# Optimization experiments

Measured on AMD Instinct MI355X. Metric: run time of the kernel, lower is better.

Reference implementation:

```python
import jax, jax.numpy as jnp
import numpy as np
from jax import lax

WINDOW_SIZE = 11
SIGMA = 1.5
C1 = 0.01 ** 2
C2 = 0.03 ** 2
EPS_DEN = 1e-12
EPS_CLAMP = 1e-6


def _gaussian_window(size=WINDOW_SIZE, sigma=SIGMA):
    xs = jnp.arange(size, dtype=jnp.float32) - size // 2
    g = jnp.exp(-(xs ** 2) / (2.0 * sigma ** 2))
    g = g / g.sum()
    w = g[:, None] * g[None, :]
    w = w / w.sum()  # already ~1; matches torch's redundant renorm
    return w  # [k, k]


def _depthwise_filter(x, window):
    # x: [B, C, H, W]; depthwise 'SAME' conv (stride 1, odd k == pad k//2)
    ch = x.shape[1]
    k = window.shape[0]
    w = jnp.broadcast_to(window[None, None], (ch, 1, k, k)).astype(x.dtype)
    return lax.conv_general_dilated(
        x, w, window_strides=(1, 1), padding='SAME',
        feature_group_count=ch,
        dimension_numbers=('NCHW', 'OIHW', 'NCHW'))


def setup_inputs() -> dict:
    key = jax.random.key(0)
    kx, ky = jax.random.split(key)
    B, C, H, W = 32, 1, 512, 512
    x = jax.random.uniform(kx, (B, C, H, W), dtype=jnp.float32)
    y = jax.random.uniform(ky, (B, C, H, W), dtype=jnp.float32)
    return {"x": x, "y": y}


def reference(x, y):
    window = _gaussian_window().astype(x.dtype)
    mu_x = _depthwise_filter(x, window)
    mu_y = _depthwise_filter(y, window)
    sigma_x = _depthwise_filter(x * x, window) - mu_x * mu_x
    sigma_y = _depthwise_filter(y * y, window) - mu_y * mu_y
    sigma_xy = _depthwise_filter(x * y, window) - mu_x * mu_y
    num = (2.0 * mu_x * mu_y + C1) * (2.0 * sigma_xy + C2)
    den = (mu_x * mu_x + mu_y * mu_y + C1) * (sigma_x + sigma_y + C2)
    ssim_map = num / (den + EPS_DEN)
    ssim_map = jnp.clip(ssim_map, -1.0 + EPS_CLAMP, 1.0 - EPS_CLAMP)
    return 1.0 - jnp.mean(ssim_map)
```

## Files before the change

kernel.cpp:

```cpp
#include <hip/hip_runtime.h>

#define IMG    512
#define TW     32
#define TH     64
#define R      5
#define KW     11
#define HB_H   (TH + 2*R)
#define HB_W   33
#define GX     (IMG / TW)
#define GY     (IMG / TH)
#define NBATCH 32
#define NB     (GX * GY * NBATCH)

#define C1f 0.0001f
#define C2f 0.0009f

__device__ __forceinline__ void make_window(float* w) {
    float s = 0.f;
#pragma unroll
    for (int i = 0; i < KW; ++i) {
        float d = (float)(i - R);
        w[i] = expf(-(d * d) * (1.0f / (2.0f * 1.5f * 1.5f)));
        s += w[i];
    }
    float inv = 1.0f / s;
#pragma unroll
    for (int i = 0; i < KW; ++i) w[i] *= inv;
}

__global__ __launch_bounds__(256, 3) void ssim_tile_kernel(
    const float* __restrict__ x, const float* __restrict__ y,
    float* __restrict__ partials)
{
    __shared__ float4 hb4[HB_H][HB_W];
    __shared__ float  hb1[HB_H][HB_W];
    __shared__ float  red[4];

    float w[KW];
    make_window(w);

    const int tc = blockIdx.x;
    const int tr = blockIdx.y;
    const int b  = blockIdx.z;
    const int tid = threadIdx.x;

    const size_t imgBase = (size_t)b * IMG * IMG;
    const int gr0 = tr * TH - R;

    for (int it = tid; it < HB_H * 8; it += 256) {
        const int rr = it >> 3;
        const int g  = it & 7;
        const int gr = gr0 + rr;
        const bool rowok = (gr >= 0) && (gr < IMG);
        const int grc = rowok ? gr : 0;
        const float4* rx = (const float4*)(x + imgBase + (size_t)grc * IMG);
        const float4* ry = (const float4*)(y + imgBase + (size_t)grc * IMG);

        const int c4 = tc * 8 + g - 2;
        float fx[20], fy[20];
#pragma unroll
        for (int i = 0; i < 5; ++i) {
            int ci = c4 + i;
            bool ok = rowok && (ci >= 0) && (ci < IMG / 4);
            int cic = min(max(ci, 0), IMG / 4 - 1);
            float4 vx = rx[cic];
            float4 vy = ry[cic];
            float m = ok ? 1.f : 0.f;
            fx[4*i+0] = vx.x * m; fx[4*i+1] = vx.y * m;
            fx[4*i+2] = vx.z * m; fx[4*i+3] = vx.w * m;
            fy[4*i+0] = vy.x * m; fy[4*i+1] = vy.y * m;
            fy[4*i+2] = vy.z * m; fy[4*i+3] = vy.w * m;
        }
        float xx[14], yy[14], xy[14];
#pragma unroll
        for (int t = 0; t < 14; ++t) {
            float px = fx[3 + t], py = fy[3 + t];
            xx[t] = px * px; yy[t] = py * py; xy[t] = px * py;
        }
#pragma unroll
        for (int k = 0; k < 4; ++k) {
            float ax = 0.f, ay = 0.f, axx = 0.f, ayy = 0.f, axy = 0.f;
#pragma unroll
            for (int t = 0; t < KW; ++t) {
                float wt = w[t];
                int j = k + t;
                ax  += wt * fx[3 + j];
                ay  += wt * fy[3 + j];
                axx += wt * xx[j];
                ayy += wt * yy[j];
                axy += wt * xy[j];
            }
            hb4[rr][4*g + k] = make_float4(ax, ay, axx, ayy);
            hb1[rr][4*g + k] = axy;
        }
    }
    __syncthreads();

    const int tx = tid & 31;
    const int ty = tid >> 5;
    const int r0 = ty * 8;

    float a0[8], a1[8], a2[8], a3[8], a4[8];
#pragma unroll
    for (int k = 0; k < 8; ++k) { a0[k]=0.f; a1[k]=0.f; a2[k]=0.f; a3[k]=0.f; a4[k]=0.f; }

#pragma unroll
    for (int t = 0; t < 18; ++t) {
        float4 v4 = hb4[r0 + t][tx];
        float  v1 = hb1[r0 + t][tx];
#pragma unroll
        for (int k = 0; k < 8; ++k) {
            if (t - k >= 0 && t - k < KW) {
                float wt = w[t - k];
                a0[k] += wt * v4.x;
                a1[k] += wt * v4.y;
                a2[k] += wt * v4.z;
                a3[k] += wt * v4.w;
                a4[k] += wt * v1;
            }
        }
    }

    float lsum = 0.f;
#pragma unroll
    for (int k = 0; k < 8; ++k) {
        float mux = a0[k], muy = a1[k];
        float sxx = a2[k] - mux * mux;
        float syy = a3[k] - muy * muy;
        float sxy = a4[k] - mux * muy;
        float num = (2.f * mux * muy + C1f) * (2.f * sxy + C2f);
        float den = (mux * mux + muy * muy + C1f) * (sxx + syy + C2f);
        float ssim = num / (den + 1e-12f);
        ssim = fminf(fmaxf(ssim, -1.f + 1e-6f), 1.f - 1e-6f);
        lsum += ssim;
    }

#pragma unroll
    for (int off = 32; off > 0; off >>= 1)
        lsum += __shfl_down(lsum, off, 64);
    if ((tid & 63) == 0) red[tid >> 6] = lsum;
    __syncthreads();
    if (tid == 0) {
        float s = red[0] + red[1] + red[2] + red[3];
        partials[((size_t)b * GY + tr) * GX + tc] = s;
    }
}

__global__ __launch_bounds__(256) void ssim_finalize(
    const float* __restrict__ partials, float* __restrict__ out)
{
    __shared__ float red[4];
    float s = 0.f;
    for (int i = threadIdx.x; i < NB; i += 256) s += partials[i];
#pragma unroll
    for (int off = 32; off > 0; off >>= 1)
        s += __shfl_down(s, off, 64);
    if ((threadIdx.x & 63) == 0) red[threadIdx.x >> 6] = s;
    __syncthreads();
    if (threadIdx.x == 0) {
        float t = red[0] + red[1] + red[2] + red[3];
        out[0] = 1.0f - t / (float)(NBATCH * IMG * IMG);
    }
}

extern "C" void kernel_launch(void* const* d_in, const int* in_sizes, int n_in,
                              void* d_out, int out_size, void* d_ws, size_t ws_size,
                              hipStream_t stream) {
    const float* x = (const float*)d_in[0];
    const float* y = (const float*)d_in[1];
    float* out = (float*)d_out;
    float* partials = (float*)d_ws;

    dim3 grid(GX, GY, NBATCH);
    dim3 block(256);
    ssim_tile_kernel<<<grid, block, 0, stream>>>(x, y, partials);
    ssim_finalize<<<1, 256, 0, stream>>>(partials, out);
}
```

Measured before the change: 131.9 us.

## Fuse finalize via atomics, shrink tile height, hardcode weights, restructure horizontal pass

Merges the finalize kernel into the tile kernel with an atomic sum and a last-block counter, and adds a memset so the workspace starts at zero. Tile height drops from 64 to 48 with row masking for the partial last tile, and occupancy is raised to 4 blocks per SM. Gaussian weights become compile-time constants. The horizontal pass now handles 8 columns per thread with fewer threads, and interior tiles skip the boundary masking. The float atomic accumulation makes the summation order nondeterministic, and the extra memset launch adds work.

```diff
diff --git a/kernel.cpp b/kernel.cpp
--- a/kernel.cpp
+++ b/kernel.cpp
@@ -2,116 +2,138 @@
 
 #define IMG    512
 #define TW     32
-#define TH     64
+#define TH     48
 #define R      5
 #define KW     11
 #define HB_H   (TH + 2*R)
-#define HB_W   33
+#define W4     33
+#define W1     36
 #define GX     (IMG / TW)
-#define GY     (IMG / TH)
+#define GY     ((IMG + TH - 1) / TH)
 #define NBATCH 32
-#define NB     (GX * GY * NBATCH)
-
+#define NBLOCKS (GX * GY * NBATCH)
 #define C1f 0.0001f
 #define C2f 0.0009f
 
-__device__ __forceinline__ void make_window(float* w) {
-    float s = 0.f;
-#pragma unroll
-    for (int i = 0; i < KW; ++i) {
-        float d = (float)(i - R);
-        w[i] = expf(-(d * d) * (1.0f / (2.0f * 1.5f * 1.5f)));
-        s += w[i];
-    }
-    float inv = 1.0f / s;
-#pragma unroll
-    for (int i = 0; i < KW; ++i) w[i] *= inv;
-}
-
-__global__ __launch_bounds__(256, 3) void ssim_tile_kernel(
+__global__ __launch_bounds__(256, 4) void ssim_fused_kernel(
     const float* __restrict__ x, const float* __restrict__ y,
-    float* __restrict__ partials)
+    float* __restrict__ out, float* __restrict__ ws)
 {
-    __shared__ float4 hb4[HB_H][HB_W];
-    __shared__ float  hb1[HB_H][HB_W];
+    __shared__ float4 hb4[HB_H][W4];
+    __shared__ float  hb1[HB_H][W1];
     __shared__ float  red[4];
 
-    float w[KW];
-    make_window(w);
+    const float W[KW] = {
+        0.00102838f, 0.00759874f, 0.03600077f, 0.10936075f, 0.21300553f,
+        0.26601172f,
+        0.21300553f, 0.10936075f, 0.03600077f, 0.00759874f, 0.00102838f};
 
-    const int tc = blockIdx.x;
-    const int tr = blockIdx.y;
-    const int b  = blockIdx.z;
+    const int tc = blockIdx.x, tr = blockIdx.y, b = blockIdx.z;
     const int tid = threadIdx.x;
+    const size_t imgBase = (size_t)b * (IMG * IMG);
+    const int gr0 = tr * TH - R;
+    const bool colEdge = (tc == 0) || (tc == GX - 1);
 
-    const size_t imgBase = (size_t)b * IMG * IMG;
-    const int gr0 = tr * TH - R;
-
-    for (int it = tid; it < HB_H * 8; it += 256) {
-        const int rr = it >> 3;
-        const int g  = it & 7;
+    if (tid < HB_H * 4) {
+        const int rr = tid >> 2;
+        const int g  = tid & 3;
         const int gr = gr0 + rr;
-        const bool rowok = (gr >= 0) && (gr < IMG);
-        const int grc = rowok ? gr : 0;
-        const float4* rx = (const float4*)(x + imgBase + (size_t)grc * IMG);
-        const float4* ry = (const float4*)(y + imgBase + (size_t)grc * IMG);
-
-        const int c4 = tc * 8 + g - 2;
-        float fx[20], fy[20];
+        float4* h4 = &hb4[rr][8 * g];
+        float*  h1 = &hb1[rr][8 * g];
+        if ((unsigned)gr < (unsigned)IMG) {
+            const float4* rx = (const float4*)(x + imgBase + (size_t)gr * IMG);
+            const float4* ry = (const float4*)(y + imgBase + (size_t)gr * IMG);
+            const int q0 = tc * 8 + 2 * g - 2;
+            float fx[24], fy[24];
+            if (colEdge) {
 #pragma unroll
-        for (int i = 0; i < 5; ++i) {
-            int ci = c4 + i;
-            bool ok = rowok && (ci >= 0) && (ci < IMG / 4);
-            int cic = min(max(ci, 0), IMG / 4 - 1);
-            float4 vx = rx[cic];
-            float4 vy = ry[cic];
-            float m = ok ? 1.f : 0.f;
-            fx[4*i+0] = vx.x * m; fx[4*i+1] = vx.y * m;
-            fx[4*i+2] = vx.z * m; fx[4*i+3] = vx.w * m;
-            fy[4*i+0] = vy.x * m; fy[4*i+1] = vy.y * m;
-            fy[4*i+2] = vy.z * m; fy[4*i+3] = vy.w * m;
-        }
-        float xx[14], yy[14], xy[14];
+                for (int i = 0; i < 6; ++i) {
+                    int q = q0 + i;
+                    int qc = min(max(q, 0), IMG / 4 - 1);
+                    float4 vx = rx[qc], vy = ry[qc];
+                    float m = (q == qc) ? 1.f : 0.f;
+                    fx[4*i+0]=vx.x*m; fx[4*i+1]=vx.y*m; fx[4*i+2]=vx.z*m; fx[4*i+3]=vx.w*m;
+                    fy[4*i+0]=vy.x*m; fy[4*i+1]=vy.y*m; fy[4*i+2]=vy.z*m; fy[4*i+3]=vy.w*m;
+                }
+            } else {
 #pragma unroll
-        for (int t = 0; t < 14; ++t) {
-            float px = fx[3 + t], py = fy[3 + t];
-            xx[t] = px * px; yy[t] = py * py; xy[t] = px * py;
-        }
+                for (int i = 0; i < 6; ++i) {
+                    float4 vx = rx[q0 + i], vy = ry[q0 + i];
+                    fx[4*i+0]=vx.x; fx[4*i+1]=vx.y; fx[4*i+2]=vx.z; fx[4*i+3]=vx.w;
+                    fy[4*i+0]=vy.x; fy[4*i+1]=vy.y; fy[4*i+2]=vy.z; fy[4*i+3]=vy.w;
+                }
+            }
+            {
+                float a0[4]={0,0,0,0}, a1[4]={0,0,0,0}, a2[4]={0,0,0,0},
+                      a3[4]={0,0,0,0}, a4[4]={0,0,0,0};
 #pragma unroll
-        for (int k = 0; k < 4; ++k) {
-            float ax = 0.f, ay = 0.f, axx = 0.f, ayy = 0.f, axy = 0.f;
+                for (int j = 3; j <= 16; ++j) {
+                    float px = fx[j], py = fy[j];
+                    float xx = px*px, yy = py*py, xy = px*py;
 #pragma unroll
-            for (int t = 0; t < KW; ++t) {
-                float wt = w[t];
-                int j = k + t;
-                ax  += wt * fx[3 + j];
-                ay  += wt * fy[3 + j];
-                axx += wt * xx[j];
-                ayy += wt * yy[j];
-                axy += wt * xy[j];
+                    for (int k = 0; k < 4; ++k) {
+                        const int t = j - 3 - k;
+                        if (t >= 0 && t < KW) {
+                            const float wt = W[t];
+                            a0[k] += wt*px; a1[k] += wt*py;
+                            a2[k] += wt*xx; a3[k] += wt*yy; a4[k] += wt*xy;
+                        }
+                    }
+                }
+#pragma unroll
+                for (int k = 0; k < 4; ++k)
+                    h4[k] = make_float4(a0[k], a1[k], a2[k], a3[k]);
+                *(float4*)h1 = make_float4(a4[0], a4[1], a4[2], a4[3]);
             }
-            hb4[rr][4*g + k] = make_float4(ax, ay, axx, ayy);
-            hb1[rr][4*g + k] = axy;
+            {
+                float a0[4]={0,0,0,0}, a1[4]={0,0,0,0}, a2[4]={0,0,0,0},
+                      a3[4]={0,0,0,0}, a4[4]={0,0,0,0};
+#pragma unroll
+                for (int j = 7; j <= 20; ++j) {
+                    float px = fx[j], py = fy[j];
+                    float xx = px*px, yy = py*py, xy = px*py;
+#pragma unroll
+                    for (int k = 0; k < 4; ++k) {
+                        const int t = j - 7 - k;
+                        if (t >= 0 && t < KW) {
+                            const float wt = W[t];
+                            a0[k] += wt*px; a1[k] += wt*py;
+                            a2[k] += wt*xx; a3[k] += wt*yy; a4[k] += wt*xy;
+                        }
+                    }
+                }
+#pragma unroll
+                for (int k = 0; k < 4; ++k)
+                    h4[4 + k] = make_float4(a0[k], a1[k], a2[k], a3[k]);
+                *(float4*)(h1 + 4) = make_float4(a4[0], a4[1], a4[2], a4[3]);
+            }
+        } else {
+            const float4 z = make_float4(0.f, 0.f, 0.f, 0.f);
+#pragma unroll
+            for (int k = 0; k < 8; ++k) h4[k] = z;
+            *(float4*)h1 = z;
+            *(float4*)(h1 + 4) = z;
         }
     }
     __syncthreads();
 
     const int tx = tid & 31;
     const int ty = tid >> 5;
-    const int r0 = ty * 8;
+    const int r0 = ty * 6;
 
-    float a0[8], a1[8], a2[8], a3[8], a4[8];
+    float a0[6], a1[6], a2[6], a3[6], a4[6];
 #pragma unroll
-    for (int k = 0; k < 8; ++k) { a0[k]=0.f; a1[k]=0.f; a2[k]=0.f; a3[k]=0.f; a4[k]=0.f; }
+    for (int k = 0; k < 6; ++k) { a0[k]=0.f; a1[k]=0.f; a2[k]=0.f; a3[k]=0.f; a4[k]=0.f; }
 
 #pragma unroll
-    for (int t = 0; t < 18; ++t) {
+    for (int t = 0; t < 16; ++t) {
         float4 v4 = hb4[r0 + t][tx];
         float  v1 = hb1[r0 + t][tx];
 #pragma unroll
-        for (int k = 0; k < 8; ++k) {
-            if (t - k >= 0 && t - k < KW) {
-                float wt = w[t - k];
+        for (int k = 0; k < 6; ++k) {
+            const int u = t - k;
+            if (u >= 0 && u < KW) {
+                const float wt = W[u];
                 a0[k] += wt * v4.x;
                 a1[k] += wt * v4.y;
                 a2[k] += wt * v4.z;
@@ -122,8 +144,9 @@
     }
 
     float lsum = 0.f;
+    const int grOut = tr * TH + r0;
 #pragma unroll
-    for (int k = 0; k < 8; ++k) {
+    for (int k = 0; k < 6; ++k) {
         float mux = a0[k], muy = a1[k];
         float sxx = a2[k] - mux * mux;
         float syy = a3[k] - muy * muy;
@@ -132,7 +155,7 @@
         float den = (mux * mux + muy * muy + C1f) * (sxx + syy + C2f);
         float ssim = num / (den + 1e-12f);
         ssim = fminf(fmaxf(ssim, -1.f + 1e-6f), 1.f - 1e-6f);
-        lsum += ssim;
+        lsum += (grOut + k < IMG) ? ssim : 0.f;
     }
 
 #pragma unroll
@@ -142,24 +165,14 @@
     __syncthreads();
     if (tid == 0) {
         float s = red[0] + red[1] + red[2] + red[3];
-        partials[((size_t)b * GY + tr) * GX + tc] = s;
-    }
-}
-
-__global__ __launch_bounds__(256) void ssim_finalize(
-    const float* __restrict__ partials, float* __restrict__ out)
-{
-    __shared__ float red[4];
-    float s = 0.f;
-    for (int i = threadIdx.x; i < NB; i += 256) s += partials[i];
-#pragma unroll
-    for (int off = 32; off > 0; off >>= 1)
-        s += __shfl_down(s, off, 64);
-    if ((threadIdx.x & 63) == 0) red[threadIdx.x >> 6] = s;
-    __syncthreads();
-    if (threadIdx.x == 0) {
-        float t = red[0] + red[1] + red[2] + red[3];
-        out[0] = 1.0f - t / (float)(NBATCH * IMG * IMG);
+        atomicAdd(&ws[0], s);
+        __threadfence();
+        unsigned old = atomicAdd((unsigned*)&ws[1], 1u);
+        if (old == (unsigned)(NBLOCKS - 1)) {
+            __threadfence();
+            float tot = atomicAdd(&ws[0], 0.0f);
+            out[0] = 1.0f - tot * (1.0f / (32.0f * 512.0f * 512.0f));
+        }
     }
 }
 
@@ -169,10 +182,9 @@
     const float* x = (const float*)d_in[0];
     const float* y = (const float*)d_in[1];
     float* out = (float*)d_out;
-    float* partials = (float*)d_ws;
+    float* ws  = (float*)d_ws;
 
+    hipMemsetAsync(d_ws, 0, 2 * sizeof(float), stream);
     dim3 grid(GX, GY, NBATCH);
-    dim3 block(256);
-    ssim_tile_kernel<<<grid, block, 0, stream>>>(x, y, partials);
-    ssim_finalize<<<1, 256, 0, stream>>>(partials, out);
+    ssim_fused_kernel<<<grid, 256, 0, stream>>>(x, y, out, ws);
 }
```

After: 275.2 us. 109% more time.
